# Kernel optimization log

Measured on AMD Instinct MI355X. Metric: run time of the kernel, lower is better.

Reference implementation:

```python
import jax, jax.numpy as jnp
import numpy as np
import math

B, L, D, H = 4, 2048, 768, 6
HD = D // H  # head_dim = 128

def setup_inputs() -> dict:
    key = jax.random.key(0)
    ks = jax.random.split(key, 9)
    s = 0.02
    return {
        "x": jax.random.normal(ks[0], (B, L, D), dtype=jnp.float32),
        "Wq": jax.random.normal(ks[1], (D, D), dtype=jnp.float32) * s,
        "bq": jnp.zeros((D,), dtype=jnp.float32),
        "Wk": jax.random.normal(ks[2], (D, D), dtype=jnp.float32) * s,
        "bk": jnp.zeros((D,), dtype=jnp.float32),
        "Wv": jax.random.normal(ks[3], (D, D), dtype=jnp.float32) * s,
        "bv": jnp.zeros((D,), dtype=jnp.float32),
        "Wo": jax.random.normal(ks[4], (D, D), dtype=jnp.float32) * s,
        "bo": jnp.zeros((D,), dtype=jnp.float32),
    }

def _split_heads(t):
    # [b, l, h*d] -> [b, h, l, d]
    b, l, _ = t.shape
    return t.reshape(b, l, H, HD).transpose(0, 2, 1, 3)

def reference(x, Wq, bq, Wk, bk, Wv, bv, Wo, bo):
    q = _split_heads(x @ Wq + bq)
    k = _split_heads(x @ Wk + bk)
    v = _split_heads(x @ Wv + bv)
    scores = jnp.einsum("bhqd,bhkd->bhqk", q, k) / math.sqrt(HD)
    # Original builds jnp.tril(ones, k=1) and fills mask==0 positions; it
    # mistakenly used +inf there, which yields NaN — we use -inf (intended
    # masking math) while keeping the same tril(k=1) pattern.
    l = x.shape[1]
    mask = jnp.tril(jnp.ones((l, l), dtype=bool), k=1)
    logits = jnp.where(mask, scores, -jnp.inf)
    attn = jax.nn.softmax(logits, axis=-1)
    out = jnp.einsum("bhqk,bhkd->bhqd", attn, v)
    out = out.transpose(0, 2, 1, 3).reshape(x.shape[0], l, D)
    # dropout in eval/deterministic mode: identity
    return out @ Wo + bo
```

## Files before the change

### kernel.cpp

```cpp
#include <hip/hip_runtime.h>
#include <math.h>

#define HEADS 6
#define SEQ   2048
#define DIM   768
#define HDIM  128
#define BATCH 4
#define MTOT  (BATCH*SEQ)
#define NKV   (SEQ/32)

typedef float  f32x4  __attribute__((ext_vector_type(4)));
typedef __bf16 bf16x8 __attribute__((ext_vector_type(8)));
typedef __bf16 bf16x4 __attribute__((ext_vector_type(4)));
typedef float  f32x4v __attribute__((ext_vector_type(4)));

typedef __attribute__((address_space(3))) void lds_v;
typedef __attribute__((address_space(1))) void gbl_v;

__device__ __forceinline__ f32x4 mfma16(bf16x8 a, bf16x8 b, f32x4 c) {
    return __builtin_amdgcn_mfma_f32_16x16x32_bf16(a, b, c, 0, 0, 0);
}
__device__ __forceinline__ unsigned int bperm(int srclane, unsigned int v) {
    return (unsigned int)__builtin_amdgcn_ds_bpermute(srclane << 2, (int)v);
}
__device__ __forceinline__ unsigned int pack2(float lo, float hi) {
    union { __bf16 b; unsigned short u; } a, c;
    a.b = (__bf16)lo; c.b = (__bf16)hi;
    return ((unsigned int)c.u << 16) | (unsigned int)a.u;
}

__global__ __launch_bounds__(256) void cast_x_kernel(const float* __restrict__ x,
                                                     __bf16* __restrict__ xb) {
    int i = (blockIdx.x * 256 + threadIdx.x) * 4;
    f32x4v v = *(const f32x4v*)(x + i);
    bf16x4 o;
    o[0] = (__bf16)v[0]; o[1] = (__bf16)v[1];
    o[2] = (__bf16)v[2]; o[3] = (__bf16)v[3];
    *(bf16x4*)(xb + i) = o;
}

__global__ __launch_bounds__(256) void transpose_w_kernel(
    const float* __restrict__ W0, const float* __restrict__ W1,
    const float* __restrict__ W2, const float* __restrict__ W3,
    __bf16* __restrict__ T0, __bf16* __restrict__ T1,
    __bf16* __restrict__ T2, __bf16* __restrict__ T3) {
    __shared__ float tile[32][33];
    const float* W; __bf16* T;
    if      (blockIdx.z == 0) { W = W0; T = T0; }
    else if (blockIdx.z == 1) { W = W1; T = T1; }
    else if (blockIdx.z == 2) { W = W2; T = T2; }
    else                      { W = W3; T = T3; }
    int n0 = blockIdx.x * 32, k0 = blockIdx.y * 32;
    int tx = threadIdx.x & 31, ty = threadIdx.x >> 5;
#pragma unroll
    for (int i = 0; i < 4; ++i)
        tile[ty + i*8][tx] = W[(size_t)(k0 + ty + i*8) * DIM + n0 + tx];
    __syncthreads();
#pragma unroll
    for (int i = 0; i < 4; ++i)
        T[(size_t)(n0 + ty + i*8) * DIM + k0 + tx] = (__bf16)tile[tx][ty + i*8];
}

__global__ __launch_bounds__(256) void gemm_qkv(const __bf16* __restrict__ A,
                                                const __bf16* __restrict__ Wcat,
                                                const float* __restrict__ bq,
                                                const float* __restrict__ bk,
                                                const float* __restrict__ bv,
                                                __bf16* __restrict__ Qb,
                                                __bf16* __restrict__ Kb,
                                                __bf16* __restrict__ Vt) {
    constexpr int KD = DIM, NT = 2304;
    __shared__ __align__(16) __bf16 As[128 * 32];
    __shared__ __align__(16) __bf16 Bs[128 * 32];
    const int tid  = threadIdx.x;
    const int wave = tid >> 6, lane = tid & 63;
    const int l16  = lane & 15, lh = lane >> 4;
    const int bn = blockIdx.x % (NT / 128), bm = blockIdx.x / (NT / 128);
    const int m0 = bm * 128, n0 = bn * 128;
    const int wr = wave >> 1, wc = wave & 1;
    f32x4 acc[4][4] = {};

    for (int k0 = 0; k0 < KD; k0 += 32) {
#pragma unroll
        for (int ci = 0; ci < 4; ++ci) {
            int c = wave * 4 + ci;
            int t = c & 7;
            int e = (t * 64 + lane) * 8;
            int r = e >> 5, kk = e & 31;
            const __bf16* gp = (c < 8) ? (A    + (size_t)(m0 + r) * KD + k0 + kk)
                                       : (Wcat + (size_t)(n0 + r) * KD + k0 + kk);
            __bf16* lp = (c < 8 ? As : Bs) + t * 512;
            __builtin_amdgcn_global_load_lds((const gbl_v*)gp, (lds_v*)lp, 16, 0, 0);
        }
        __syncthreads();
        bf16x8 af[4], bfr[4];
#pragma unroll
        for (int i = 0; i < 4; ++i)
            af[i] = *(const bf16x8*)&As[(wr*64 + i*16 + l16) * 32 + lh*8];
#pragma unroll
        for (int j = 0; j < 4; ++j)
            bfr[j] = *(const bf16x8*)&Bs[(wc*64 + j*16 + l16) * 32 + lh*8];
#pragma unroll
        for (int i = 0; i < 4; ++i)
#pragma unroll
            for (int j = 0; j < 4; ++j)
                acc[i][j] = mfma16(af[i], bfr[j], acc[i][j]);
        __syncthreads();
    }

    const int sel = n0 / DIM;
    const float* bias = sel == 0 ? bq : (sel == 1 ? bk : bv);
#pragma unroll
    for (int i = 0; i < 4; ++i) {
        int row = m0 + wr*64 + i*16 + lh*4;
#pragma unroll
        for (int j = 0; j < 4; ++j) {
            int col  = n0 + wc*64 + j*16 + l16;
            int lcol = col - sel * DIM;
            float bvv = bias[lcol];
            if (sel < 2) {
                __bf16* o = (sel == 0) ? Qb : Kb;
#pragma unroll
                for (int r = 0; r < 4; ++r)
                    o[(size_t)(row + r) * DIM + lcol] = (__bf16)(acc[i][j][r] + bvv);
            } else {
                int bb = row >> 11, ll = row & (SEQ - 1);
                int hh = lcol >> 7, dd = lcol & (HDIM - 1);
                bf16x4 pk;
#pragma unroll
                for (int r = 0; r < 4; ++r) pk[r] = (__bf16)(acc[i][j][r] + bvv);
                *(bf16x4*)&Vt[((size_t)((bb*HEADS + hh) * HDIM + dd)) * SEQ + ll] = pk;
            }
        }
    }
}

__global__ __launch_bounds__(256) void gemm_out(const __bf16* __restrict__ A,
                                                const __bf16* __restrict__ Bt,
                                                const float* __restrict__ bias,
                                                float* __restrict__ outp) {
    constexpr int KD = DIM, N = DIM;
    __shared__ __align__(16) __bf16 As[128 * 32];
    __shared__ __align__(16) __bf16 Bs[128 * 32];
    const int tid  = threadIdx.x;
    const int wave = tid >> 6, lane = tid & 63;
    const int l16  = lane & 15, lh = lane >> 4;
    const int bn = blockIdx.x % (N / 128), bm = blockIdx.x / (N / 128);
    const int m0 = bm * 128, n0 = bn * 128;
    const int wr = wave >> 1, wc = wave & 1;
    f32x4 acc[4][4] = {};

    for (int k0 = 0; k0 < KD; k0 += 32) {
#pragma unroll
        for (int ci = 0; ci < 4; ++ci) {
            int c = wave * 4 + ci;
            int t = c & 7;
            int e = (t * 64 + lane) * 8;
            int r = e >> 5, kk = e & 31;
            const __bf16* gp = (c < 8) ? (A  + (size_t)(m0 + r) * KD + k0 + kk)
                                       : (Bt + (size_t)(n0 + r) * KD + k0 + kk);
            __bf16* lp = (c < 8 ? As : Bs) + t * 512;
            __builtin_amdgcn_global_load_lds((const gbl_v*)gp, (lds_v*)lp, 16, 0, 0);
        }
        __syncthreads();
        bf16x8 af[4], bfr[4];
#pragma unroll
        for (int i = 0; i < 4; ++i)
            af[i] = *(const bf16x8*)&As[(wr*64 + i*16 + l16) * 32 + lh*8];
#pragma unroll
        for (int j = 0; j < 4; ++j)
            bfr[j] = *(const bf16x8*)&Bs[(wc*64 + j*16 + l16) * 32 + lh*8];
#pragma unroll
        for (int i = 0; i < 4; ++i)
#pragma unroll
            for (int j = 0; j < 4; ++j)
                acc[i][j] = mfma16(af[i], bfr[j], acc[i][j]);
        __syncthreads();
    }

#pragma unroll
    for (int i = 0; i < 4; ++i) {
        int row = m0 + wr*64 + i*16 + lh*4;
#pragma unroll
        for (int j = 0; j < 4; ++j) {
            int col = n0 + wc*64 + j*16 + l16;
            float bv = bias[col];
#pragma unroll
            for (int r = 0; r < 4; ++r)
                outp[(size_t)(row + r) * N + col] = acc[i][j][r] + bv;
        }
    }
}

__global__ __launch_bounds__(256, 3) void attn_kernel(
    const __bf16* __restrict__ Q, const __bf16* __restrict__ K,
    const __bf16* __restrict__ Vt,
    __bf16* __restrict__ po, float* __restrict__ pm, float* __restrict__ pl,
    __bf16* __restrict__ Ob, int ks) {
    __shared__ __align__(16) __bf16 Ks[2][32 * 128];
    __shared__ __align__(16) __bf16 Vs[2][128 * 32];
    const int lane = threadIdx.x & 63, wv = threadIdx.x >> 6;
    const int l16 = lane & 15, lh = lane >> 4;
    const int id  = blockIdx.x;
    const int xcd = id & 7;
    const int idx = id >> 3;
    const int bh_l = idx % 3, rem = idx / 3;
    const int c = rem % ks, tl = rem / ks;
    const int tile = (tl & 1) ? (31 - (tl >> 1)) : (tl >> 1);
    const int bh = xcd + 8 * bh_l;
    const int b = bh / HEADS, h = bh - b * HEADS;
    const int qw0 = tile * 64 + wv * 16;
    const float qs = 0.12751674770951932f;

    bf16x8 qf[4];
    {
        const __bf16* qp = Q + (size_t)(b*SEQ + qw0 + l16) * DIM + h*HDIM + lh*8;
#pragma unroll
        for (int kk = 0; kk < 4; ++kk) {
            bf16x8 v = *(const bf16x8*)(qp + kk*32);
            bf16x8 sv;
#pragma unroll
            for (int e = 0; e < 8; ++e) sv[e] = (__bf16)((float)v[e] * qs);
            qf[kk] = sv;
        }
    }

    const __bf16* kgb = K  + (size_t)(b*SEQ) * DIM + h*HDIM;
    const __bf16* vgb = Vt + (size_t)bh * HDIM * SEQ;

    auto stage = [&](int buf, int kb) {
        const int kbase = kb * 32;
#pragma unroll
        for (int s = 0; s < 4; ++s) {
            const int j = wv * 4 + s;
            if (j < 8) {
                const int row = j * 4 + (lane >> 4);
                const int c16 = (lane & 15) ^ (row & 7);
                const __bf16* gp = kgb + (size_t)(kbase + row) * DIM + c16 * 8;
                __builtin_amdgcn_global_load_lds((const gbl_v*)gp,
                    (lds_v*)&Ks[buf][j * 512], 16, 0, 0);
            } else {
                const int jj = j - 8;
                const int row = jj * 16 + (lane >> 2);
                const int c16 = (lane & 3) ^ ((row >> 1) & 3);
                const __bf16* gp = vgb + (size_t)row * SEQ + kbase + c16 * 8;
                __builtin_amdgcn_global_load_lds((const gbl_v*)gp,
                    (lds_v*)&Vs[buf][jj * 512], 16, 0, 0);
            }
        }
    };

    f32x4 o[8] = {};
    float mx = -INFINITY, lsum = 0.f;
    const int nkb = min(2 * tile + 3, NKV);
    const int cnt = (nkb - c + ks - 1) / ks;

    stage(0, c);
    asm volatile("s_waitcnt vmcnt(0)" ::: "memory");
    __builtin_amdgcn_s_barrier();

    int cur = 0;
    for (int i = 0; i < cnt; ++i) {
        const int kb = c + i * ks;
        const int kbase = kb * 32;
        const bool more = (i + 1 < cnt);
        if (more) {
            stage(cur ^ 1, kb + ks);
            asm volatile("s_waitcnt vmcnt(4)" ::: "memory");
        } else {
            asm volatile("s_waitcnt vmcnt(0)" ::: "memory");
        }
        __builtin_amdgcn_s_barrier();

        if (kbase <= qw0 + 16) {
            bf16x8 kfA[4], kfB[4];
#pragma unroll
            for (int kk = 0; kk < 4; ++kk) {
                const int ca = (kk*4 + lh) ^ (l16 & 7);
                kfA[kk] = *(const bf16x8*)&Ks[cur][l16 * 128 + ca * 8];
                const int rb = 16 + l16;
                const int cb = (kk*4 + lh) ^ (rb & 7);
                kfB[kk] = *(const bf16x8*)&Ks[cur][rb * 128 + cb * 8];
            }
            f32x4 sA = {}, sB = {};
            __builtin_amdgcn_s_setprio(1);
#pragma unroll
            for (int kk = 0; kk < 4; ++kk) {
                sA = mfma16(kfA[kk], qf[kk], sA);
                sB = mfma16(kfB[kk], qf[kk], sB);
            }
            __builtin_amdgcn_s_setprio(0);
            const int q = qw0 + l16;
            float p[8];
#pragma unroll
            for (int r = 0; r < 4; ++r) { p[r] = sA[r]; p[r+4] = sB[r]; }
            if (kbase + 30 > qw0) {
#pragma unroll
                for (int r = 0; r < 4; ++r) {
                    const int key = kbase + lh*4 + r;
                    if (key      > q + 1) p[r]   = -INFINITY;
                    if (key + 16 > q + 1) p[r+4] = -INFINITY;
                }
            }
            float m0 = p[0];
#pragma unroll
            for (int t2 = 1; t2 < 8; ++t2) m0 = fmaxf(m0, p[t2]);
            m0 = fmaxf(m0, __shfl_xor(m0, 16));
            m0 = fmaxf(m0, __shfl_xor(m0, 32));
            const float mnew = fmaxf(mx, m0);
            const bool grow = m0 > mx;
            const float mref = (mnew == -INFINITY) ? 0.f : mnew;
#pragma unroll
            for (int t2 = 0; t2 < 8; ++t2) p[t2] = exp2f(p[t2] - mref);
            float rs = 0.f;
#pragma unroll
            for (int t2 = 0; t2 < 8; ++t2) rs += p[t2];
            rs += __shfl_xor(rs, 16);
            rs += __shfl_xor(rs, 32);
            if (__any(grow)) {
                const float resc = (mx < mnew) ? exp2f(mx - mnew) : 1.0f;
                lsum = lsum * resc + rs;
                mx = mnew;
#pragma unroll
                for (int d = 0; d < 8; ++d)
#pragma unroll
                    for (int r = 0; r < 4; ++r) o[d][r] *= resc;
            } else {
                lsum += rs;
            }
            unsigned int w0 = pack2(p[0], p[1]);
            unsigned int w1 = pack2(p[2], p[3]);
            unsigned int w2 = pack2(p[4], p[5]);
            unsigned int w3 = pack2(p[6], p[7]);
            const int s0l = l16 + ((lh & 1) << 5);
            unsigned int A0 = bperm(s0l,      w0), A1 = bperm(s0l,      w1);
            unsigned int A2 = bperm(s0l,      w2), A3 = bperm(s0l,      w3);
            unsigned int B0 = bperm(s0l + 16, w0), B1 = bperm(s0l + 16, w1);
            unsigned int B2 = bperm(s0l + 16, w2), B3 = bperm(s0l + 16, w3);
            const bool hi = (lh >= 2);
            union { unsigned int u[4]; bf16x8 v; } pu;
            pu.u[0] = hi ? A2 : A0;
            pu.u[1] = hi ? A3 : A1;
            pu.u[2] = hi ? B2 : B0;
            pu.u[3] = hi ? B3 : B1;
            const bf16x8 pf = pu.v;
            __builtin_amdgcn_s_setprio(1);
#pragma unroll
            for (int d = 0; d < 8; ++d) {
                const int row = d * 16 + l16;
                const int cv = lh ^ ((row >> 1) & 3);
                bf16x8 vf = *(const bf16x8*)&Vs[cur][row * 32 + cv * 8];
                o[d] = mfma16(vf, pf, o[d]);
            }
            __builtin_amdgcn_s_setprio(0);
        }
        __builtin_amdgcn_s_barrier();
        cur ^= 1;
    }

    if (ks == 1) {
        const float inv = 1.0f / lsum;
        __bf16* op = Ob + (size_t)(b*SEQ + qw0 + l16) * DIM + h*HDIM;
#pragma unroll
        for (int d = 0; d < 8; ++d) {
            bf16x4 pk;
#pragma unroll
            for (int r = 0; r < 4; ++r) pk[r] = (__bf16)(o[d][r] * inv);
            *(bf16x4*)(op + d*16 + lh*4) = pk;
        }
    } else {
        const int pid = (bh * 32 + tile) * ks + c;
        const int lq  = wv * 16 + l16;
        __bf16* pop = po + ((size_t)pid * 64 + lq) * HDIM;
#pragma unroll
        for (int d = 0; d < 8; ++d) {
            bf16x4 pk;
#pragma unroll
            for (int r = 0; r < 4; ++r) pk[r] = (__bf16)o[d][r];
            *(bf16x4*)(pop + d*16 + lh*4) = pk;
        }
        if (lh == 0) {
            pm[(size_t)pid * 64 + lq] = mx;
            pl[(size_t)pid * 64 + lq] = lsum;
        }
    }
}

__global__ __launch_bounds__(256) void merge_kernel(const __bf16* __restrict__ po,
    const float* __restrict__ pm, const float* __restrict__ pl,
    __bf16* __restrict__ Ob, int ks) {
    const int id = blockIdx.x;
    const int bh = id >> 5, tile = id & 31;
    const int b = bh / HEADS, h = bh - b * HEADS;
    const int lq = threadIdx.x >> 2;
    const int d0 = (threadIdx.x & 3) * 32;
    const int pb = id * ks;
    float M = -INFINITY;
    for (int cc = 0; cc < ks; ++cc) M = fmaxf(M, pm[(size_t)(pb + cc) * 64 + lq]);
    float L = 0.f, w[2] = {0.f, 0.f};
    for (int cc = 0; cc < ks; ++cc) {
        w[cc] = exp2f(pm[(size_t)(pb + cc) * 64 + lq] - M);
        L += w[cc] * pl[(size_t)(pb + cc) * 64 + lq];
    }
    const float invL = 1.0f / L;
    __bf16* op = Ob + (size_t)(b*SEQ + tile*64 + lq) * DIM + h*HDIM;
#pragma unroll
    for (int d = 0; d < 32; d += 8) {
        float acc[8] = {};
        for (int cc = 0; cc < ks; ++cc) {
            bf16x8 v = *(const bf16x8*)&po[((size_t)(pb + cc) * 64 + lq) * HDIM + d0 + d];
            const float wc = w[cc];
#pragma unroll
            for (int e = 0; e < 8; ++e) acc[e] += wc * (float)v[e];
        }
        bf16x8 ov;
#pragma unroll
        for (int e = 0; e < 8; ++e) ov[e] = (__bf16)(acc[e] * invL);
        *(bf16x8*)(op + d0 + d) = ov;
    }
}

extern "C" void kernel_launch(void* const* d_in, const int* in_sizes, int n_in,
                              void* d_out, int out_size, void* d_ws, size_t ws_size,
                              hipStream_t stream) {
    const float* x  = (const float*)d_in[0];
    const float* Wq = (const float*)d_in[1];
    const float* bq = (const float*)d_in[2];
    const float* Wk = (const float*)d_in[3];
    const float* bk = (const float*)d_in[4];
    const float* Wv = (const float*)d_in[5];
    const float* bv = (const float*)d_in[6];
    const float* Wo = (const float*)d_in[7];
    const float* bo = (const float*)d_in[8];

    char* p = (char*)d_ws;
    const size_t SZ_X = (size_t)MTOT * DIM * 2;
    const size_t SZ_W = (size_t)DIM * DIM * 2;
    __bf16* xb   = (__bf16*)p; p += SZ_X;
    __bf16* Wcat = (__bf16*)p; p += 3 * SZ_W;
    __bf16* Wto  = (__bf16*)p; p += SZ_W;
    __bf16* Qb   = (__bf16*)p; p += SZ_X;
    __bf16* Kb   = (__bf16*)p; p += SZ_X;
    __bf16* Vt   = (__bf16*)p; p += SZ_X;
    __bf16* Ob   = (__bf16*)p; p += SZ_X;

    const size_t base = (size_t)(p - (char*)d_ws);
    const size_t SZ_PO = (size_t)24 * 32 * 2 * 64 * HDIM * 2;
    const size_t SZ_PM = (size_t)24 * 32 * 2 * 64 * 4;
    const int ks = (ws_size >= base + SZ_PO + 2 * SZ_PM) ? 2 : 1;
    __bf16* po = (__bf16*)p;            p += SZ_PO;
    float*  pmv = (float*)p;            p += SZ_PM;
    float*  plv = (float*)p;

    cast_x_kernel<<<(MTOT * DIM) / 1024, 256, 0, stream>>>(x, xb);
    transpose_w_kernel<<<dim3(DIM/32, DIM/32, 4), 256, 0, stream>>>(
        Wq, Wk, Wv, Wo,
        Wcat, Wcat + (size_t)DIM*DIM, Wcat + (size_t)2*DIM*DIM, Wto);

    gemm_qkv<<<(MTOT/128) * (2304/128), 256, 0, stream>>>(xb, Wcat, bq, bk, bv, Qb, Kb, Vt);

    attn_kernel<<<768 * ks, 256, 0, stream>>>(Qb, Kb, Vt, po, pmv, plv, Ob, ks);
    if (ks == 2)
        merge_kernel<<<24 * 32, 256, 0, stream>>>(po, pmv, plv, Ob, ks);

    gemm_out<<<(MTOT/128) * (DIM/128), 256, 0, stream>>>(Ob, Wto, bo, (float*)d_out);
}
```

Before: 185.0 us.

## Triple-buffer GEMMs, shrink attention tiles, read V from global, defer rescaling

Both GEMMs switch to a shared macro that keeps three LDS buffers and prefetches two k-steps ahead, waiting with partial vmcnt instead of a full sync each step. The attention kernel drops to 128-thread blocks with 32-query tiles, doubling the block count. It also stops staging V in LDS and loads V fragments straight from global memory. Online-softmax rescaling is skipped while the running max stays within a threshold. These changes aim to hide load latency and improve load balance, but risk uncoalesced V reads and more K traffic across the smaller tiles.

```diff
diff --git a/kernel.cpp b/kernel.cpp
--- a/kernel.cpp
+++ b/kernel.cpp
@@ -61,6 +61,53 @@
         T[(size_t)(n0 + ty + i*8) * DIM + k0 + tx] = (__bf16)tile[tx][ty + i*8];
 }
 
+#define GEMM_PIPE(A_PTR, B_PTR, NKSTEP)                                           \
+    __shared__ __align__(16) __bf16 As[3][128 * 32];                              \
+    __shared__ __align__(16) __bf16 Bs[3][128 * 32];                              \
+    const int tid  = threadIdx.x;                                                 \
+    const int wave = tid >> 6, lane = tid & 63;                                   \
+    const int l16  = lane & 15, lh = lane >> 4;                                   \
+    const int wr = wave >> 1, wc = wave & 1;                                      \
+    f32x4 acc[4][4] = {};                                                         \
+    auto stage = [&](int buf, int step) {                                         \
+        const int k0 = step * 32;                                                 \
+        _Pragma("unroll")                                                         \
+        for (int ci = 0; ci < 4; ++ci) {                                          \
+            int c = wave * 4 + ci;                                                \
+            int t = c & 7;                                                        \
+            int e = (t * 64 + lane) * 8;                                          \
+            int r = e >> 5, kk = e & 31;                                          \
+            const __bf16* gp = (c < 8) ? ((A_PTR) + (size_t)(m0 + r) * DIM + k0 + kk) \
+                                       : ((B_PTR) + (size_t)(n0 + r) * DIM + k0 + kk); \
+            __bf16* lp = (c < 8 ? As[buf] : Bs[buf]) + t * 512;                   \
+            __builtin_amdgcn_global_load_lds((const gbl_v*)gp, (lds_v*)lp, 16, 0, 0); \
+        }                                                                         \
+    };                                                                            \
+    stage(0, 0); stage(1, 1);                                                     \
+    asm volatile("s_waitcnt vmcnt(4)" ::: "memory");                              \
+    __builtin_amdgcn_s_barrier();                                                 \
+    for (int t = 0; t < (NKSTEP); ++t) {                                          \
+        const int cur = t % 3;                                                    \
+        if (t + 2 < (NKSTEP)) stage((t + 2) % 3, t + 2);                          \
+        bf16x8 af[4], bfr[4];                                                     \
+        _Pragma("unroll")                                                         \
+        for (int i = 0; i < 4; ++i)                                               \
+            af[i] = *(const bf16x8*)&As[cur][(wr*64 + i*16 + l16) * 32 + lh*8];   \
+        _Pragma("unroll")                                                         \
+        for (int j = 0; j < 4; ++j)                                               \
+            bfr[j] = *(const bf16x8*)&Bs[cur][(wc*64 + j*16 + l16) * 32 + lh*8];  \
+        __builtin_amdgcn_s_setprio(1);                                            \
+        _Pragma("unroll")                                                         \
+        for (int i = 0; i < 4; ++i)                                               \
+            _Pragma("unroll")                                                     \
+            for (int j = 0; j < 4; ++j)                                           \
+                acc[i][j] = mfma16(af[i], bfr[j], acc[i][j]);                     \
+        __builtin_amdgcn_s_setprio(0);                                            \
+        if (t + 2 < (NKSTEP))      asm volatile("s_waitcnt vmcnt(4)" ::: "memory"); \
+        else if (t + 1 < (NKSTEP)) asm volatile("s_waitcnt vmcnt(0)" ::: "memory"); \
+        __builtin_amdgcn_s_barrier();                                             \
+    }
+
 __global__ __launch_bounds__(256) void gemm_qkv(const __bf16* __restrict__ A,
                                                 const __bf16* __restrict__ Wcat,
                                                 const float* __restrict__ bq,
@@ -69,44 +116,9 @@
                                                 __bf16* __restrict__ Qb,
                                                 __bf16* __restrict__ Kb,
                                                 __bf16* __restrict__ Vt) {
-    constexpr int KD = DIM, NT = 2304;
-    __shared__ __align__(16) __bf16 As[128 * 32];
-    __shared__ __align__(16) __bf16 Bs[128 * 32];
-    const int tid  = threadIdx.x;
-    const int wave = tid >> 6, lane = tid & 63;
-    const int l16  = lane & 15, lh = lane >> 4;
-    const int bn = blockIdx.x % (NT / 128), bm = blockIdx.x / (NT / 128);
+    const int bn = blockIdx.x % (2304 / 128), bm = blockIdx.x / (2304 / 128);
     const int m0 = bm * 128, n0 = bn * 128;
-    const int wr = wave >> 1, wc = wave & 1;
-    f32x4 acc[4][4] = {};
-
-    for (int k0 = 0; k0 < KD; k0 += 32) {
-#pragma unroll
-        for (int ci = 0; ci < 4; ++ci) {
-            int c = wave * 4 + ci;
-            int t = c & 7;
-            int e = (t * 64 + lane) * 8;
-            int r = e >> 5, kk = e & 31;
-            const __bf16* gp = (c < 8) ? (A    + (size_t)(m0 + r) * KD + k0 + kk)
-                                       : (Wcat + (size_t)(n0 + r) * KD + k0 + kk);
-            __bf16* lp = (c < 8 ? As : Bs) + t * 512;
-            __builtin_amdgcn_global_load_lds((const gbl_v*)gp, (lds_v*)lp, 16, 0, 0);
-        }
-        __syncthreads();
-        bf16x8 af[4], bfr[4];
-#pragma unroll
-        for (int i = 0; i < 4; ++i)
-            af[i] = *(const bf16x8*)&As[(wr*64 + i*16 + l16) * 32 + lh*8];
-#pragma unroll
-        for (int j = 0; j < 4; ++j)
-            bfr[j] = *(const bf16x8*)&Bs[(wc*64 + j*16 + l16) * 32 + lh*8];
-#pragma unroll
-        for (int i = 0; i < 4; ++i)
-#pragma unroll
-            for (int j = 0; j < 4; ++j)
-                acc[i][j] = mfma16(af[i], bfr[j], acc[i][j]);
-        __syncthreads();
-    }
+    GEMM_PIPE(A, Wcat, 24)
 
     const int sel = n0 / DIM;
     const float* bias = sel == 0 ? bq : (sel == 1 ? bk : bv);
@@ -139,44 +151,9 @@
                                                 const __bf16* __restrict__ Bt,
                                                 const float* __restrict__ bias,
                                                 float* __restrict__ outp) {
-    constexpr int KD = DIM, N = DIM;
-    __shared__ __align__(16) __bf16 As[128 * 32];
-    __shared__ __align__(16) __bf16 Bs[128 * 32];
-    const int tid  = threadIdx.x;
-    const int wave = tid >> 6, lane = tid & 63;
-    const int l16  = lane & 15, lh = lane >> 4;
-    const int bn = blockIdx.x % (N / 128), bm = blockIdx.x / (N / 128);
+    const int bn = blockIdx.x % (DIM / 128), bm = blockIdx.x / (DIM / 128);
     const int m0 = bm * 128, n0 = bn * 128;
-    const int wr = wave >> 1, wc = wave & 1;
-    f32x4 acc[4][4] = {};
-
-    for (int k0 = 0; k0 < KD; k0 += 32) {
-#pragma unroll
-        for (int ci = 0; ci < 4; ++ci) {
-            int c = wave * 4 + ci;
-            int t = c & 7;
-            int e = (t * 64 + lane) * 8;
-            int r = e >> 5, kk = e & 31;
-            const __bf16* gp = (c < 8) ? (A  + (size_t)(m0 + r) * KD + k0 + kk)
-                                       : (Bt + (size_t)(n0 + r) * KD + k0 + kk);
-            __bf16* lp = (c < 8 ? As : Bs) + t * 512;
-            __builtin_amdgcn_global_load_lds((const gbl_v*)gp, (lds_v*)lp, 16, 0, 0);
-        }
-        __syncthreads();
-        bf16x8 af[4], bfr[4];
-#pragma unroll
-        for (int i = 0; i < 4; ++i)
-            af[i] = *(const bf16x8*)&As[(wr*64 + i*16 + l16) * 32 + lh*8];
-#pragma unroll
-        for (int j = 0; j < 4; ++j)
-            bfr[j] = *(const bf16x8*)&Bs[(wc*64 + j*16 + l16) * 32 + lh*8];
-#pragma unroll
-        for (int i = 0; i < 4; ++i)
-#pragma unroll
-            for (int j = 0; j < 4; ++j)
-                acc[i][j] = mfma16(af[i], bfr[j], acc[i][j]);
-        __syncthreads();
-    }
+    GEMM_PIPE(A, Bt, 24)
 
 #pragma unroll
     for (int i = 0; i < 4; ++i) {
@@ -187,18 +164,17 @@
             float bv = bias[col];
 #pragma unroll
             for (int r = 0; r < 4; ++r)
-                outp[(size_t)(row + r) * N + col] = acc[i][j][r] + bv;
-        }
-    }
-}
-
-__global__ __launch_bounds__(256, 3) void attn_kernel(
+                outp[(size_t)(row + r) * DIM + col] = acc[i][j][r] + bv;
+        }
+    }
+}
+
+__global__ __launch_bounds__(128, 4) void attn_kernel(
     const __bf16* __restrict__ Q, const __bf16* __restrict__ K,
     const __bf16* __restrict__ Vt,
     __bf16* __restrict__ po, float* __restrict__ pm, float* __restrict__ pl,
     __bf16* __restrict__ Ob, int ks) {
     __shared__ __align__(16) __bf16 Ks[2][32 * 128];
-    __shared__ __align__(16) __bf16 Vs[2][128 * 32];
     const int lane = threadIdx.x & 63, wv = threadIdx.x >> 6;
     const int l16 = lane & 15, lh = lane >> 4;
     const int id  = blockIdx.x;
@@ -206,10 +182,10 @@
     const int idx = id >> 3;
     const int bh_l = idx % 3, rem = idx / 3;
     const int c = rem % ks, tl = rem / ks;
-    const int tile = (tl & 1) ? (31 - (tl >> 1)) : (tl >> 1);
+    const int tile = (tl & 1) ? (63 - (tl >> 1)) : (tl >> 1);
     const int bh = xcd + 8 * bh_l;
     const int b = bh / HEADS, h = bh - b * HEADS;
-    const int qw0 = tile * 64 + wv * 16;
+    const int qw0 = tile * 32 + wv * 16;
     const float qs = 0.12751674770951932f;
 
     bf16x8 qf[4];
@@ -233,26 +209,17 @@
 #pragma unroll
         for (int s = 0; s < 4; ++s) {
             const int j = wv * 4 + s;
-            if (j < 8) {
-                const int row = j * 4 + (lane >> 4);
-                const int c16 = (lane & 15) ^ (row & 7);
-                const __bf16* gp = kgb + (size_t)(kbase + row) * DIM + c16 * 8;
-                __builtin_amdgcn_global_load_lds((const gbl_v*)gp,
-                    (lds_v*)&Ks[buf][j * 512], 16, 0, 0);
-            } else {
-                const int jj = j - 8;
-                const int row = jj * 16 + (lane >> 2);
-                const int c16 = (lane & 3) ^ ((row >> 1) & 3);
-                const __bf16* gp = vgb + (size_t)row * SEQ + kbase + c16 * 8;
-                __builtin_amdgcn_global_load_lds((const gbl_v*)gp,
-                    (lds_v*)&Vs[buf][jj * 512], 16, 0, 0);
-            }
+            const int row = j * 4 + (lane >> 4);
+            const int c16 = (lane & 15) ^ (row & 7);
+            const __bf16* gp = kgb + (size_t)(kbase + row) * DIM + c16 * 8;
+            __builtin_amdgcn_global_load_lds((const gbl_v*)gp,
+                (lds_v*)&Ks[buf][j * 512], 16, 0, 0);
         }
     };
 
     f32x4 o[8] = {};
     float mx = -INFINITY, lsum = 0.f;
-    const int nkb = min(2 * tile + 3, NKV);
+    const int nkb = min(tile + 2, NKV);
     const int cnt = (nkb - c + ks - 1) / ks;
 
     stage(0, c);
@@ -263,8 +230,7 @@
     for (int i = 0; i < cnt; ++i) {
         const int kb = c + i * ks;
         const int kbase = kb * 32;
-        const bool more = (i + 1 < cnt);
-        if (more) {
+        if (i + 1 < cnt) {
             stage(cur ^ 1, kb + ks);
             asm volatile("s_waitcnt vmcnt(4)" ::: "memory");
         } else {
@@ -290,6 +256,12 @@
                 sB = mfma16(kfB[kk], qf[kk], sB);
             }
             __builtin_amdgcn_s_setprio(0);
+            bf16x8 vf[8];
+            const __bf16* vrow = vgb + kbase + lh * 8;
+#pragma unroll
+            for (int d = 0; d < 8; ++d)
+                vf[d] = *(const bf16x8*)(vrow + (size_t)(d*16 + l16) * SEQ);
+
             const int q = qw0 + l16;
             float p[8];
 #pragma unroll
@@ -307,9 +279,18 @@
             for (int t2 = 1; t2 < 8; ++t2) m0 = fmaxf(m0, p[t2]);
             m0 = fmaxf(m0, __shfl_xor(m0, 16));
             m0 = fmaxf(m0, __shfl_xor(m0, 32));
-            const float mnew = fmaxf(mx, m0);
-            const bool grow = m0 > mx;
-            const float mref = (mnew == -INFINITY) ? 0.f : mnew;
+            const bool defer = __all(m0 <= mx + 8.f && mx > -3e38f);
+            if (!defer) {
+                const float mnew = fmaxf(mx, m0);
+                const float resc = (mx < mnew) ? exp2f(mx - mnew) : 1.0f;
+                lsum *= resc;
+#pragma unroll
+                for (int d = 0; d < 8; ++d)
+#pragma unroll
+                    for (int r = 0; r < 4; ++r) o[d][r] *= resc;
+                mx = mnew;
+            }
+            const float mref = (mx == -INFINITY) ? 0.f : mx;
 #pragma unroll
             for (int t2 = 0; t2 < 8; ++t2) p[t2] = exp2f(p[t2] - mref);
             float rs = 0.f;
@@ -317,17 +298,7 @@
             for (int t2 = 0; t2 < 8; ++t2) rs += p[t2];
             rs += __shfl_xor(rs, 16);
             rs += __shfl_xor(rs, 32);
-            if (__any(grow)) {
-                const float resc = (mx < mnew) ? exp2f(mx - mnew) : 1.0f;
-                lsum = lsum * resc + rs;
-                mx = mnew;
-#pragma unroll
-                for (int d = 0; d < 8; ++d)
-#pragma unroll
-                    for (int r = 0; r < 4; ++r) o[d][r] *= resc;
-            } else {
-                lsum += rs;
-            }
+            lsum += rs;
             unsigned int w0 = pack2(p[0], p[1]);
             unsigned int w1 = pack2(p[2], p[3]);
             unsigned int w2 = pack2(p[4], p[5]);
@@ -346,12 +317,8 @@
             const bf16x8 pf = pu.v;
             __builtin_amdgcn_s_setprio(1);
 #pragma unroll
-            for (int d = 0; d < 8; ++d) {
-                const int row = d * 16 + l16;
-                const int cv = lh ^ ((row >> 1) & 3);
-                bf16x8 vf = *(const bf16x8*)&Vs[cur][row * 32 + cv * 8];
-                o[d] = mfma16(vf, pf, o[d]);
-            }
+            for (int d = 0; d < 8; ++d)
+                o[d] = mfma16(vf[d], pf, o[d]);
             __builtin_amdgcn_s_setprio(0);
         }
         __builtin_amdgcn_s_barrier();
@@ -369,9 +336,9 @@
             *(bf16x4*)(op + d*16 + lh*4) = pk;
         }
     } else {
-        const int pid = (bh * 32 + tile) * ks + c;
+        const int pid = (bh * 64 + tile) * ks + c;
         const int lq  = wv * 16 + l16;
-        __bf16* pop = po + ((size_t)pid * 64 + lq) * HDIM;
+        __bf16* pop = po + ((size_t)pid * 32 + lq) * HDIM;
 #pragma unroll
         for (int d = 0; d < 8; ++d) {
             bf16x4 pk;
@@ -380,35 +347,35 @@
             *(bf16x4*)(pop + d*16 + lh*4) = pk;
         }
         if (lh == 0) {
-            pm[(size_t)pid * 64 + lq] = mx;
-            pl[(size_t)pid * 64 + lq] = lsum;
-        }
-    }
-}
-
-__global__ __launch_bounds__(256) void merge_kernel(const __bf16* __restrict__ po,
+            pm[(size_t)pid * 32 + lq] = mx;
+            pl[(size_t)pid * 32 + lq] = lsum;
+        }
+    }
+}
+
+__global__ __launch_bounds__(128) void merge_kernel(const __bf16* __restrict__ po,
     const float* __restrict__ pm, const float* __restrict__ pl,
     __bf16* __restrict__ Ob, int ks) {
     const int id = blockIdx.x;
-    const int bh = id >> 5, tile = id & 31;
+    const int bh = id >> 6, tile = id & 63;
     const int b = bh / HEADS, h = bh - b * HEADS;
     const int lq = threadIdx.x >> 2;
     const int d0 = (threadIdx.x & 3) * 32;
     const int pb = id * ks;
     float M = -INFINITY;
-    for (int cc = 0; cc < ks; ++cc) M = fmaxf(M, pm[(size_t)(pb + cc) * 64 + lq]);
+    for (int cc = 0; cc < ks; ++cc) M = fmaxf(M, pm[(size_t)(pb + cc) * 32 + lq]);
     float L = 0.f, w[2] = {0.f, 0.f};
     for (int cc = 0; cc < ks; ++cc) {
-        w[cc] = exp2f(pm[(size_t)(pb + cc) * 64 + lq] - M);
-        L += w[cc] * pl[(size_t)(pb + cc) * 64 + lq];
+        w[cc] = exp2f(pm[(size_t)(pb + cc) * 32 + lq] - M);
+        L += w[cc] * pl[(size_t)(pb + cc) * 32 + lq];
     }
     const float invL = 1.0f / L;
-    __bf16* op = Ob + (size_t)(b*SEQ + tile*64 + lq) * DIM + h*HDIM;
+    __bf16* op = Ob + (size_t)(b*SEQ + tile*32 + lq) * DIM + h*HDIM;
 #pragma unroll
     for (int d = 0; d < 32; d += 8) {
         float acc[8] = {};
         for (int cc = 0; cc < ks; ++cc) {
-            bf16x8 v = *(const bf16x8*)&po[((size_t)(pb + cc) * 64 + lq) * HDIM + d0 + d];
+            bf16x8 v = *(const bf16x8*)&po[((size_t)(pb + cc) * 32 + lq) * HDIM + d0 + d];
             const float wc = w[cc];
 #pragma unroll
             for (int e = 0; e < 8; ++e) acc[e] += wc * (float)v[e];
@@ -445,8 +412,8 @@
     __bf16* Ob   = (__bf16*)p; p += SZ_X;
 
     const size_t base = (size_t)(p - (char*)d_ws);
-    const size_t SZ_PO = (size_t)24 * 32 * 2 * 64 * HDIM * 2;
-    const size_t SZ_PM = (size_t)24 * 32 * 2 * 64 * 4;
+    const size_t SZ_PO = (size_t)24 * 64 * 2 * 32 * HDIM * 2;
+    const size_t SZ_PM = (size_t)24 * 64 * 2 * 32 * 4;
     const int ks = (ws_size >= base + SZ_PO + 2 * SZ_PM) ? 2 : 1;
     __bf16* po = (__bf16*)p;            p += SZ_PO;
     float*  pmv = (float*)p;            p += SZ_PM;
@@ -459,9 +426,9 @@
 
     gemm_qkv<<<(MTOT/128) * (2304/128), 256, 0, stream>>>(xb, Wcat, bq, bk, bv, Qb, Kb, Vt);
 
-    attn_kernel<<<768 * ks, 256, 0, stream>>>(Qb, Kb, Vt, po, pmv, plv, Ob, ks);
+    attn_kernel<<<8 * 3 * 64 * ks, 128, 0, stream>>>(Qb, Kb, Vt, po, pmv, plv, Ob, ks);
     if (ks == 2)
-        merge_kernel<<<24 * 32, 256, 0, stream>>>(po, pmv, plv, Ob, ks);
+        merge_kernel<<<24 * 64, 128, 0, stream>>>(po, pmv, plv, Ob, ks);
 
     gemm_out<<<(MTOT/128) * (DIM/128), 256, 0, stream>>>(Ob, Wto, bo, (float*)d_out);
 }
```

Measured after the change: 245.5 us. +32.7%, slower.
